# Kernel optimization log

Measured on AMD Instinct MI355X. Metric: run time of the kernel, lower is better.

## Reference

```python
import math
import jax, jax.numpy as jnp
from jax import lax
import numpy as np

NUM_EXPERTS = 8
TOP_K = 2
CAPACITY_FACTOR = 1.25
AUX_COEF = 0.01


def setup_inputs() -> dict:
    key = jax.random.key(0)
    k1, k2, k3, k4, k5 = jax.random.split(key, 5)
    B, T, C, I, E = 4, 2048, 768, 3072, NUM_EXPERTS
    x = jax.random.normal(k1, (B, T, C), dtype=jnp.float32)
    Wr = jax.random.normal(k2, (C, E), dtype=jnp.float32) * 0.02
    Wg = jax.random.normal(k3, (E, C, I), dtype=jnp.float32) * 0.02
    Wu = jax.random.normal(k4, (E, C, I), dtype=jnp.float32) * 0.02
    Wp = jax.random.normal(k5, (E, I, C), dtype=jnp.float32) * 0.02
    return {"x": x, "Wr": Wr, "Wg": Wg, "Wu": Wu, "Wp": Wp}


def reference(x, Wr, Wg, Wu, Wp):
    E, K = NUM_EXPERTS, TOP_K
    B, T, C = x.shape
    N = B * T
    capacity = max(1, math.ceil(CAPACITY_FACTOR * N / E))  # static: 1280
    xf = x.reshape(N, C)

    # --- router ---
    logits = xf @ Wr                                    # [N, E]
    probs = jax.nn.softmax(logits.astype(jnp.float32), axis=-1)
    gates, idx = lax.top_k(probs, K)                    # [N, 2] each
    gates = gates / jnp.clip(jnp.sum(gates, axis=-1, keepdims=True), 1e-9)

    # --- aux load-balancing loss ---
    oh1 = jax.nn.one_hot(idx[:, 0], E, dtype=jnp.int32)  # [N, E]
    oh2 = jax.nn.one_hot(idx[:, 1], E, dtype=jnp.int32)
    importance = probs.mean(axis=0)
    load = (oh1 + oh2).astype(jnp.float32).mean(axis=0) / K
    aux_loss = jnp.sum(importance * load) * E * AUX_COEF

    # --- capacity positions (running rank within each expert) ---
    pos1 = jnp.sum((jnp.cumsum(oh1, axis=0) - 1) * oh1, axis=-1)   # [N]
    mask1 = pos1 < capacity
    slot1 = idx[:, 0] * capacity + pos1
    count1 = jnp.minimum(jnp.sum(oh1, axis=0), capacity)           # [E]
    pos2 = jnp.sum((jnp.cumsum(oh2, axis=0) - 1) * oh2, axis=-1) + count1[idx[:, 1]]
    mask2 = pos2 < capacity
    slot2 = idx[:, 1] * capacity + pos2

    # --- dispatch (scatter into per-expert buffers; OOB slots dropped) ---
    buf = jnp.zeros((E * capacity, C), dtype=x.dtype)
    s1 = jnp.where(mask1, slot1, E * capacity)
    s2 = jnp.where(mask2, slot2, E * capacity)
    buf = buf.at[s1].set(xf, mode='drop')
    buf = buf.at[s2].set(xf, mode='drop')
    ein = buf.reshape(E, capacity, C)

    # --- per-expert swiglu MLP (grouped GEMMs) ---
    gate = jax.nn.silu(jnp.einsum('enc,ech->enh', ein, Wg))
    up = jnp.einsum('enc,ech->enh', ein, Wu)
    out = jnp.einsum('enh,ehc->enc', gate * up, Wp).reshape(E * capacity, C)

    # --- combine (gather back to token order, renormalized gates) ---
    g1 = gates[:, 0] * mask1.astype(jnp.float32)
    g2 = gates[:, 1] * mask2.astype(jnp.float32)
    denom = jnp.clip(g1 + g2, 1e-9)
    g1 = (g1 / denom).astype(x.dtype)
    g2 = (g2 / denom).astype(x.dtype)
    c1 = jnp.clip(slot1, 0, E * capacity - 1)
    c2 = jnp.clip(slot2, 0, E * capacity - 1)
    y = g1[:, None] * out[c1] + g2[:, None] * out[c2]
    return y.reshape(B, T, C), aux_loss
```

## Files before the change

### kernel.cpp

```cpp
#include <hip/hip_runtime.h>
#include <cstdint>
#include <cstddef>

#define NTOK 8192
#define NEXP 8
#define CAP 1280
#define CDIM 768
#define IDIM 3072
#define EROWS (NEXP*CAP)

typedef __attribute__((ext_vector_type(8))) short short8;
typedef __attribute__((ext_vector_type(4))) float f32x4;
typedef __attribute__((ext_vector_type(4))) unsigned short us4;
typedef __attribute__((ext_vector_type(8))) unsigned short us8;

__device__ __forceinline__ unsigned short f2b(float f) {
  unsigned u = __builtin_bit_cast(unsigned, f);
  u += 0x7FFFu + ((u >> 16) & 1u);
  return (unsigned short)(u >> 16);
}
__device__ __forceinline__ float b2f(unsigned short u) {
  return __builtin_bit_cast(float, ((unsigned)u) << 16);
}

__global__ __launch_bounds__(256) void transpose_cvt64(const float* __restrict__ src,
    unsigned short* __restrict__ dst, int R, int S) {
  int tilesS = S >> 6, tilesR = R >> 6;
  int perE = tilesR * tilesS;
  int e = blockIdx.x / perE;
  int rem = blockIdx.x % perE;
  int rt = rem / tilesS, st = rem % tilesS;
  const float* se = src + (size_t)e*R*S + ((size_t)rt*64)*S + st*64;
  unsigned short* de = dst + (size_t)e*R*S + ((size_t)st*64)*R + rt*64;
  __shared__ float tile[64][65];
  int c4 = (threadIdx.x & 15)*4, rr = threadIdx.x >> 4;
#pragma unroll
  for (int p = 0; p < 4; ++p) {
    float4 v = *(const float4*)(se + (size_t)(rr + 16*p)*S + c4);
    tile[rr + 16*p][c4+0] = v.x; tile[rr + 16*p][c4+1] = v.y;
    tile[rr + 16*p][c4+2] = v.z; tile[rr + 16*p][c4+3] = v.w;
  }
  __syncthreads();
#pragma unroll
  for (int p = 0; p < 4; ++p) {
    int s = rr + 16*p;
    us4 o;
    o.x = f2b(tile[c4+0][s]); o.y = f2b(tile[c4+1][s]);
    o.z = f2b(tile[c4+2][s]); o.w = f2b(tile[c4+3][s]);
    *(us4*)(de + (size_t)s*R + c4) = o;
  }
}

__global__ __launch_bounds__(256) void wgu_cvt64(const float* __restrict__ Wg,
    const float* __restrict__ Wu, unsigned short* __restrict__ Wgu) {
  const int tilesR = CDIM/64, tilesS = IDIM/64;
  const int perE = tilesR * tilesS;
  int sel = blockIdx.x / (NEXP*perE);
  int rem = blockIdx.x % (NEXP*perE);
  int e = rem / perE; int r2 = rem % perE;
  int rt = r2 / tilesS, st = r2 % tilesS;
  const float* se = (sel ? Wu : Wg) + (size_t)e*CDIM*IDIM + ((size_t)rt*64)*IDIM + st*64;
  __shared__ float tile[64][65];
  int c4 = (threadIdx.x & 15)*4, rr = threadIdx.x >> 4;
#pragma unroll
  for (int p = 0; p < 4; ++p) {
    float4 v = *(const float4*)(se + (size_t)(rr + 16*p)*IDIM + c4);
    tile[rr + 16*p][c4+0] = v.x; tile[rr + 16*p][c4+1] = v.y;
    tile[rr + 16*p][c4+2] = v.z; tile[rr + 16*p][c4+3] = v.w;
  }
  __syncthreads();
  unsigned short* dstE = Wgu + (size_t)e*(2*IDIM)*CDIM;
#pragma unroll
  for (int p = 0; p < 4; ++p) {
    int s = rr + 16*p;
    int np = 128*st + 32*(s>>4) + (s&15) + sel*16;
    us4 o;
    o.x = f2b(tile[c4+0][s]); o.y = f2b(tile[c4+1][s]);
    o.z = f2b(tile[c4+2][s]); o.w = f2b(tile[c4+3][s]);
    *(us4*)(dstE + (size_t)np*CDIM + rt*64 + c4) = o;
  }
}

__global__ __launch_bounds__(256) void router_kernel(const float* __restrict__ x,
    const float* __restrict__ Wr, float* __restrict__ probs,
    int* __restrict__ idx1, int* __restrict__ idx2,
    float* __restrict__ g1r, float* __restrict__ g2r) {
  __shared__ float WrT[NEXP*CDIM];
  for (int i = threadIdx.x; i < NEXP*CDIM; i += 256) {
    int c = i >> 3, e = i & 7;
    WrT[e*CDIM + c] = Wr[i];
  }
  __syncthreads();
  int w = threadIdx.x >> 6, l = threadIdx.x & 63;
  int t = blockIdx.x*4 + w;
  float acc[NEXP];
#pragma unroll
  for (int e = 0; e < NEXP; ++e) acc[e] = 0.f;
  for (int k = 0; k < CDIM/64; ++k) {
    float xv = x[(size_t)t*CDIM + k*64 + l];
#pragma unroll
    for (int e = 0; e < NEXP; ++e) acc[e] += xv * WrT[e*CDIM + k*64 + l];
  }
#pragma unroll
  for (int off = 32; off > 0; off >>= 1) {
#pragma unroll
    for (int e = 0; e < NEXP; ++e) acc[e] += __shfl_xor(acc[e], off);
  }
  if (l == 0) {
    float m = acc[0];
#pragma unroll
    for (int e = 1; e < NEXP; ++e) m = fmaxf(m, acc[e]);
    float p[NEXP]; float s = 0.f;
#pragma unroll
    for (int e = 0; e < NEXP; ++e) { p[e] = expf(acc[e] - m); s += p[e]; }
    float inv = 1.f / s;
#pragma unroll
    for (int e = 0; e < NEXP; ++e) { p[e] *= inv; probs[(size_t)t*NEXP + e] = p[e]; }
    int i1 = 0; float b1 = p[0];
#pragma unroll
    for (int e = 1; e < NEXP; ++e) if (p[e] > b1) { b1 = p[e]; i1 = e; }
    int i2 = -1; float b2 = -1e30f;
#pragma unroll
    for (int e = 0; e < NEXP; ++e) if (e != i1 && p[e] > b2) { b2 = p[e]; i2 = e; }
    float gs = fmaxf(b1 + b2, 1e-9f);
    g1r[t] = b1 / gs; g2r[t] = b2 / gs;
    idx1[t] = i1; idx2[t] = i2;
  }
}

__global__ __launch_bounds__(1024) void scan_kernel(
    const int* __restrict__ idx1, const int* __restrict__ idx2,
    const float* __restrict__ g1r, const float* __restrict__ g2r,
    const float* __restrict__ probs,
    int* __restrict__ bufmap,
    int* __restrict__ c1o, int* __restrict__ c2o,
    float* __restrict__ g1o, float* __restrict__ g2o,
    float* __restrict__ aux_out) {
  __shared__ unsigned int scanbuf[1024][9];
  __shared__ unsigned int totals[NEXP];
  int tid = threadIdx.x;
  int e1[8], e2[8];
  unsigned int cnt[NEXP];
#pragma unroll
  for (int k = 0; k < NEXP; ++k) cnt[k] = 0;
  for (int j = 0; j < 8; ++j) {
    int t = tid*8 + j;
    e1[j] = idx1[t]; e2[j] = idx2[t];
    cnt[e1[j]] += 1u;
    cnt[e2[j]] += (1u << 16);
  }
#pragma unroll
  for (int k = 0; k < NEXP; ++k) scanbuf[tid][k] = cnt[k];
  unsigned int run[NEXP];
#pragma unroll
  for (int k = 0; k < NEXP; ++k) run[k] = cnt[k];
  __syncthreads();
  for (int off = 1; off < 1024; off <<= 1) {
    unsigned int add[NEXP];
#pragma unroll
    for (int k = 0; k < NEXP; ++k) add[k] = 0;
    if (tid >= off) {
#pragma unroll
      for (int k = 0; k < NEXP; ++k) add[k] = scanbuf[tid - off][k];
    }
    __syncthreads();
#pragma unroll
    for (int k = 0; k < NEXP; ++k) { run[k] += add[k]; scanbuf[tid][k] = run[k]; }
    __syncthreads();
  }
  if (tid == 1023) {
#pragma unroll
    for (int k = 0; k < NEXP; ++k) totals[k] = run[k];
  }
  __syncthreads();
  unsigned int excl[NEXP];
#pragma unroll
  for (int k = 0; k < NEXP; ++k) excl[k] = run[k] - cnt[k];
  int cnt1c[NEXP];
#pragma unroll
  for (int k = 0; k < NEXP; ++k) cnt1c[k] = min((int)(totals[k] & 0xFFFFu), CAP);

  for (int j = 0; j < 8; ++j) {
    int t = tid*8 + j;
    int a = e1[j];
    int pos1 = (int)(excl[a] & 0xFFFFu); excl[a] += 1u;
    int slot1 = a*CAP + pos1;
    bool m1 = pos1 < CAP;
    if (m1) bufmap[slot1] = t;
    int b = e2[j];
    int pos2 = (int)(excl[b] >> 16) + cnt1c[b]; excl[b] += (1u << 16);
    int slot2 = b*CAP + pos2;
    bool m2 = pos2 < CAP;
    if (m2) bufmap[slot2] = t;
    float G1 = m1 ? g1r[t] : 0.f;
    float G2 = m2 ? g2r[t] : 0.f;
    float den = fmaxf(G1 + G2, 1e-9f);
    g1o[t] = G1 / den; g2o[t] = G2 / den;
    c1o[t] = min(slot1, EROWS - 1);
    c2o[t] = min(slot2, EROWS - 1);
  }

  float imp[NEXP];
#pragma unroll
  for (int k = 0; k < NEXP; ++k) imp[k] = 0.f;
  for (int j = 0; j < 8; ++j) {
    int t = tid*8 + j;
    const float4* pr = (const float4*)(probs + (size_t)t*NEXP);
    float4 a0 = pr[0], a1 = pr[1];
    imp[0] += a0.x; imp[1] += a0.y; imp[2] += a0.z; imp[3] += a0.w;
    imp[4] += a1.x; imp[5] += a1.y; imp[6] += a1.z; imp[7] += a1.w;
  }
  __syncthreads();
  float* fbuf = (float*)&scanbuf[0][0];
#pragma unroll
  for (int k = 0; k < NEXP; ++k) fbuf[tid*9 + k] = imp[k];
  __syncthreads();
  for (int s = 512; s >= 1; s >>= 1) {
    if (tid < s) {
#pragma unroll
      for (int k = 0; k < NEXP; ++k) fbuf[tid*9 + k] += fbuf[(tid + s)*9 + k];
    }
    __syncthreads();
  }
  if (tid == 0) {
    float aux = 0.f;
#pragma unroll
    for (int k = 0; k < NEXP; ++k) {
      float importance = fbuf[k] / (float)NTOK;
      float loadk = (float)((totals[k] & 0xFFFFu) + (totals[k] >> 16)) / ((float)NTOK * 2.0f);
      aux += importance * loadk;
    }
    aux_out[0] = aux * (float)NEXP * 0.01f;
  }
}

__global__ __launch_bounds__(192) void dispatch_kernel(const float* __restrict__ x,
    const int* __restrict__ bufmap, unsigned short* __restrict__ ein) {
  int r = blockIdx.x;
  int t = bufmap[r];
  int q = threadIdx.x;
  float4 v = make_float4(0.f, 0.f, 0.f, 0.f);
  if (t >= 0) v = ((const float4*)x)[(size_t)t*(CDIM/4) + q];
  us4 o;
  o.x = f2b(v.x); o.y = f2b(v.y); o.z = f2b(v.z); o.w = f2b(v.w);
  ((us4*)ein)[(size_t)r*(CDIM/4) + q] = o;
}

#define BAR  asm volatile("s_barrier" ::: "memory")
#define VMW(N) asm volatile("s_waitcnt vmcnt(" #N ")" ::: "memory")
#define LGW  asm volatile("s_waitcnt lgkmcnt(0)" ::: "memory")
#define P1 __builtin_amdgcn_s_setprio(1)
#define P0 __builtin_amdgcn_s_setprio(0)

template<int KD>
__global__ __launch_bounds__(512, 2) void gemm1_8ph(
    const unsigned short* __restrict__ A,
    const unsigned short* __restrict__ Bw,
    unsigned short* __restrict__ H) {
  __shared__ unsigned short lds[81920];
  constexpr size_t JSTR = (size_t)6*256*KD;

  const int bid = blockIdx.x;
  const int chunk = gridDim.x >> 3;
  const int tile = (bid & 7)*chunk + (bid >> 3);
  const int e = tile / 30;
  const int r30 = tile % 30;
  const int ntb = r30 / 5, mt = r30 % 5;

  const int tid = threadIdx.x;
  const int l = tid & 63, wid = tid >> 6;
  const int wr = wid >> 2, wc = wid & 3;
  const int lrow = l & 15, khi = l >> 4;

  const unsigned short* Ab = A  + (size_t)e*CAP*KD      + (size_t)mt*256*KD;
  const unsigned short* Bb = Bw + (size_t)e*(2*IDIM)*KD + (size_t)ntb*256*KD;

  const int srow = tid >> 3;
  const int scol = (tid & 7) ^ (srow & 7);
  const size_t lane_off = (size_t)srow*KD + scol*8;
  const int lds_st = wid*512;

#define STG(dstu, srcp, half, kt) do { \
    const unsigned short* s_ = (srcp) + lane_off + (size_t)(half)*128*KD + (size_t)(kt)*64; \
    unsigned short* d_ = (unsigned short*)lds + (dstu) + (half)*8192 + lds_st; \
    __builtin_amdgcn_global_load_lds((const __attribute__((address_space(1))) void*)s_, \
        (__attribute__((address_space(3))) void*)d_, 16, 0, 0); \
    __builtin_amdgcn_global_load_lds((const __attribute__((address_space(1))) void*)(s_ + (size_t)64*KD), \
        (__attribute__((address_space(3))) void*)(d_ + 4096), 16, 0, 0); \
  } while(0)

  const int swz0 = ((khi    ) ^ (lrow & 7)) * 8;
  const int swz1 = ((4 + khi) ^ (lrow & 7)) * 8;
  const int aoff = wr*8192 + lrow*64;
  const int boff = (wc>>1)*8192 + ((wc&1)*64 + lrow)*64;

#define LDA(ab, dst, mb) do { _Pragma("unroll") for (int m_=0;m_<4;++m_) { \
    dst[m_][0] = *(const short8*)(lds + (ab) + aoff + ((mb)+m_)*1024 + swz0); \
    dst[m_][1] = *(const short8*)(lds + (ab) + aoff + ((mb)+m_)*1024 + swz1); } } while(0)
#define LDB(bb, dst, nb) do { _Pragma("unroll") for (int n_=0;n_<2;++n_) { \
    dst[n_][0] = *(const short8*)(lds + (bb) + boff + ((nb)+n_)*1024 + swz0); \
    dst[n_][1] = *(const short8*)(lds + (bb) + boff + ((nb)+n_)*1024 + swz1); } } while(0)
#define QUAD(af, bf, mb, nb) do { _Pragma("unroll") for (int r_=0;r_<2;++r_) \
    _Pragma("unroll") for (int n_=0;n_<2;++n_) \
    _Pragma("unroll") for (int m_=0;m_<4;++m_) \
      acc[(mb)+m_][(nb)+n_] = __builtin_amdgcn_mfma_f32_16x16x32_bf16(af[m_][r_], bf[n_][r_], acc[(mb)+m_][(nb)+n_], 0,0,0); } while(0)

  f32x4 acc[8][4];
#pragma unroll
  for (int i = 0; i < 8; ++i)
#pragma unroll
    for (int j = 0; j < 4; ++j) acc[i][j] = (f32x4){0.f,0.f,0.f,0.f};

  short8 a[4][2], bl[2][2], bh[2][2];

  int bA_ = 32768, bB_ = 49152, bC_ = 65536;

  STG(0, Ab, 0, 0);      STG(bA_, Bb, 0, 0);
  STG(0, Ab, 1, 0);      STG(bA_, Bb, 1, 0);
  STG(16384, Ab, 0, 1);  STG(bB_, Bb, 0, 1);
  STG(16384, Ab, 1, 1);  STG(bB_, Bb, 1, 1);
  VMW(8);
  BAR;

#define ITER(k2p, B2) \
    LDA(0, a, 0); LDB(bA_, bl, 0); STG(bC_, (B2), 0, (k2p)); \
    BAR; P1; QUAD(a, bl, 0, 0); P0; BAR; \
    LDB(bA_, bh, 2); STG(bC_, (B2), 1, (k2p)); \
    BAR; P1; QUAD(a, bh, 0, 2); P0; BAR; \
    LDA(0, a, 4); \
    BAR; P1; QUAD(a, bh, 4, 2); P0; BAR; \
    STG(0, Ab, 0, (k2p)); VMW(6); \
    BAR; P1; QUAD(a, bl, 4, 0); P0; BAR; \
    LDA(16384, a, 0); LDB(bB_, bl, 0); STG(0, Ab, 1, (k2p)); STG(bA_, (B2), 0, (k2p)+1); \
    BAR; P1; QUAD(a, bl, 0, 0); P0; BAR; \
    LDB(bB_, bh, 2); STG(bA_, (B2), 1, (k2p)+1); \
    BAR; P1; QUAD(a, bh, 0, 2); P0; BAR; \
    LDA(16384, a, 4); \
    BAR; P1; QUAD(a, bh, 4, 2); P0; BAR; \
    STG(16384, Ab, 0, (k2p)+1); STG(16384, Ab, 1, (k2p)+1); VMW(8); \
    BAR; P1; QUAD(a, bl, 4, 0); P0; BAR;

  const size_t rowg = (size_t)e*CAP + (size_t)mt*256;
  int itr = 0;

#pragma unroll 1
  for (int j = 0; j < 4; ++j) {
#pragma unroll 1
    for (int ii = 0; ii < 6; ++ii) {
      int t2 = 2*itr + 2;
      if (t2 >= 48) t2 = 0;
      int j2 = t2 / 12, k2 = t2 - j2*12;
      const unsigned short* B2 = Bb + (size_t)j2*JSTR;
      ITER(k2, B2);
      int tmp = bC_; bC_ = bB_; bB_ = bA_; bA_ = tmp;
      ++itr;
    }
    {
      const size_t ntcol = (size_t)(ntb + 6*j)*128;
#pragma unroll
      for (int c = 0; c < 4; ++c) {
        BAR;
        if (wr == (c >> 1)) {
#pragma unroll
          for (int m_ = 0; m_ < 4; ++m_) {
#pragma unroll
            for (int p = 0; p < 2; ++p) {
              f32x4 g = acc[(c & 1)*4 + m_][2*p], u = acc[(c & 1)*4 + m_][2*p+1];
#pragma unroll
              for (int r = 0; r < 4; ++r) {
                float gv = g[r];
                float hv = gv / (1.f + __expf(-gv)) * u[r];
                lds[bC_ + (m_*16 + khi*4 + r)*136 + wc*32 + lrow + p*16] = f2b(hv);
              }
            }
          }
        }
        LGW;
        BAR;
#pragma unroll
        for (int q = 0; q < 2; ++q) {
          int idx = tid + 512*q;
          int rp = idx >> 4, ch = idx & 15;
          us8 v = *(const us8*)(lds + bC_ + rp*136 + ch*8);
          *(us8*)(H + (rowg + 64*c + rp)*(size_t)IDIM + ntcol + ch*8) = v;
        }
      }
      BAR;
    }
#pragma unroll
    for (int i2 = 0; i2 < 8; ++i2)
#pragma unroll
      for (int j2 = 0; j2 < 4; ++j2) acc[i2][j2] = (f32x4){0.f,0.f,0.f,0.f};
  }

#undef ITER
#undef QUAD
#undef LDB
#undef LDA
#undef STG
}

template<int KD>
__global__ __launch_bounds__(512, 2) void gemm2_8ph(
    const unsigned short* __restrict__ A,
    const unsigned short* __restrict__ Bw,
    unsigned short* __restrict__ O) {
  constexpr int NT = KD/64;
  constexpr int NITER = NT/2;
  __shared__ unsigned short lds[57344];

  const int bid = blockIdx.x;
  const int chunk = gridDim.x >> 3;
  const int tile = (bid & 7)*chunk + (bid >> 3);
  const int e = tile / 30;
  const int rem = tile % 30;
  const int nt = rem / 5, mt = rem % 5;

  const int tid = threadIdx.x;
  const int l = tid & 63, wid = tid >> 6;
  const int wr = wid >> 1, wc = wid & 1;
  const int lrow = l & 15, khi = l >> 4;

  const unsigned short* Ab = A  + (size_t)e*CAP*KD  + (size_t)mt*256*KD;
  const unsigned short* Bb = Bw + (size_t)e*CDIM*KD + (size_t)nt*128*KD;

  const int srow = tid >> 3;
  const int scol = (tid & 7) ^ (srow & 7);
  const size_t lane_off = (size_t)srow*KD + scol*8;
  const int lds_st = wid*512;

#define STG(dstu, srcp, half, kt) do { \
    const unsigned short* s_ = (srcp) + lane_off + (size_t)(half)*128*KD + (size_t)(kt)*64; \
    unsigned short* d_ = (unsigned short*)lds + (dstu) + (half)*8192 + lds_st; \
    __builtin_amdgcn_global_load_lds((const __attribute__((address_space(1))) void*)s_, \
        (__attribute__((address_space(3))) void*)d_, 16, 0, 0); \
    __builtin_amdgcn_global_load_lds((const __attribute__((address_space(1))) void*)(s_ + (size_t)64*KD), \
        (__attribute__((address_space(3))) void*)(d_ + 4096), 16, 0, 0); \
  } while(0)

  const int swz0 = ((khi    ) ^ (lrow & 7)) * 8;
  const int swz1 = ((4 + khi) ^ (lrow & 7)) * 8;
  const int aoff = wr*4096 + lrow*64;
  const int boff = wc*4096 + lrow*64;

#define LDA(ab, dst) do { _Pragma("unroll") for (int m_=0;m_<4;++m_) { \
    dst[m_][0] = *(const short8*)(lds + (ab) + aoff + m_*1024 + swz0); \
    dst[m_][1] = *(const short8*)(lds + (ab) + aoff + m_*1024 + swz1); } } while(0)
#define LDB(bb, dst, nb) do { _Pragma("unroll") for (int n_=0;n_<2;++n_) { \
    dst[n_][0] = *(const short8*)(lds + (bb) + boff + ((nb)+n_)*1024 + swz0); \
    dst[n_][1] = *(const short8*)(lds + (bb) + boff + ((nb)+n_)*1024 + swz1); } } while(0)
#define QUAD(af, bf, nb) do { _Pragma("unroll") for (int r_=0;r_<2;++r_) \
    _Pragma("unroll") for (int n_=0;n_<2;++n_) \
    _Pragma("unroll") for (int m_=0;m_<4;++m_) \
      acc[m_][(nb)+n_] = __builtin_amdgcn_mfma_f32_16x16x32_bf16(af[m_][r_], bf[n_][r_], acc[m_][(nb)+n_], 0,0,0); } while(0)

  f32x4 acc[4][4];
#pragma unroll
  for (int i = 0; i < 4; ++i)
#pragma unroll
    for (int j = 0; j < 4; ++j) acc[i][j] = (f32x4){0.f,0.f,0.f,0.f};

  short8 a[4][2], bl[2][2], bh[2][2];

  int bA_ = 32768, bB_ = 40960, bC_ = 49152;

  STG(0, Ab, 0, 0); STG(0, Ab, 1, 0); STG(bA_, Bb, 0, 0);
  STG(16384, Ab, 0, 1); STG(16384, Ab, 1, 1); STG(bB_, Bb, 0, 1);
  VMW(6);
  BAR;

#define ITER2(t2, t3, DOS, VM2, VM4) \
    LDA(0, a); LDB(bA_, bl, 0); if (DOS) STG(bC_, Bb, 0, (t2)); \
    BAR; P1; QUAD(a, bl, 0); P0; BAR; \
    LDB(bA_, bh, 2); if (DOS) { STG(0, Ab, 0, (t2)); STG(0, Ab, 1, (t2)); } VM2; \
    BAR; P1; QUAD(a, bh, 2); P0; BAR; \
    LDA(16384, a); LDB(bB_, bl, 0); if (DOS) STG(bA_, Bb, 0, (t3)); \
    BAR; P1; QUAD(a, bl, 0); P0; BAR; \
    LDB(bB_, bh, 2); if (DOS) { STG(16384, Ab, 0, (t3)); STG(16384, Ab, 1, (t3)); } VM4; \
    BAR; P1; QUAD(a, bh, 2); P0; BAR;

#pragma unroll 1
  for (int i = 0; i < NITER-1; ++i) {
    const int t2 = 2*i+2, t3 = 2*i+3;
    ITER2(t2, t3, true, VMW(6), VMW(6));
    int tmp = bC_; bC_ = bB_; bB_ = bA_; bA_ = tmp;
  }
  ITER2(0, 0, false, VMW(0), VMW(0));

#undef ITER2
#undef QUAD
#undef LDB
#undef LDA
#undef STG

  __syncthreads();
  {
    const int cb0 = wc*64 + lrow;
    const int rb0 = wr*64 + khi*4;
#pragma unroll
    for (int m = 0; m < 4; ++m)
#pragma unroll
      for (int n = 0; n < 4; ++n) {
        f32x4 v = acc[m][n];
#pragma unroll
        for (int r = 0; r < 4; ++r)
          lds[(rb0 + m*16 + r)*136 + cb0 + n*16] = f2b(v[r]);
      }
  }
  __syncthreads();
  const size_t rowg = (size_t)e*CAP + (size_t)mt*256;
  const size_t colg = (size_t)nt*128 + (size_t)(l & 15)*8;
#pragma unroll
  for (int i = 0; i < 8; ++i) {
    int row = wid*32 + i*4 + (l >> 4);
    us8 v = *(const us8*)(lds + row*136 + (l & 15)*8);
    *(us8*)(O + (rowg + row)*(size_t)CDIM + colg) = v;
  }
}

__global__ __launch_bounds__(192) void combine_kernel(const unsigned short* __restrict__ outbuf,
    const int* __restrict__ c1, const int* __restrict__ c2,
    const float* __restrict__ g1, const float* __restrict__ g2,
    float* __restrict__ y) {
  int t = blockIdx.x;
  int q = threadIdx.x;
  float f1 = g1[t], f2 = g2[t];
  int a = c1[t], b = c2[t];
  us4 va = ((const us4*)outbuf)[(size_t)a*(CDIM/4) + q];
  us4 vb = ((const us4*)outbuf)[(size_t)b*(CDIM/4) + q];
  float4 r;
  r.x = f1*b2f(va.x) + f2*b2f(vb.x);
  r.y = f1*b2f(va.y) + f2*b2f(vb.y);
  r.z = f1*b2f(va.z) + f2*b2f(vb.z);
  r.w = f1*b2f(va.w) + f2*b2f(vb.w);
  ((float4*)y)[(size_t)t*(CDIM/4) + q] = r;
}

extern "C" void kernel_launch(void* const* d_in, const int* in_sizes, int n_in,
                              void* d_out, int out_size, void* d_ws, size_t ws_size,
                              hipStream_t stream) {
  const float* x  = (const float*)d_in[0];
  const float* Wr = (const float*)d_in[1];
  const float* Wg = (const float*)d_in[2];
  const float* Wu = (const float*)d_in[3];
  const float* Wp = (const float*)d_in[4];
  float* y = (float*)d_out;

  char* p = (char*)d_ws;
  auto alloc = [&](size_t bytes) { char* r = p; p += (bytes + 255) & ~(size_t)255; return r; };
  unsigned short* WguT = (unsigned short*)alloc((size_t)NEXP*2*IDIM*CDIM*2);
  unsigned short* WpT  = (unsigned short*)alloc((size_t)NEXP*CDIM*IDIM*2);
  unsigned short* ein  = (unsigned short*)alloc((size_t)EROWS*CDIM*2);
  unsigned short* h    = (unsigned short*)alloc((size_t)EROWS*IDIM*2);
  unsigned short* outbuf = (unsigned short*)alloc((size_t)EROWS*CDIM*2);
  float* probs  = (float*)alloc((size_t)NTOK*NEXP*4);
  int* idx1 = (int*)alloc(NTOK*4);
  int* idx2 = (int*)alloc(NTOK*4);
  int* c1   = (int*)alloc(NTOK*4);
  int* c2   = (int*)alloc(NTOK*4);
  float* g1r = (float*)alloc(NTOK*4);
  float* g2r = (float*)alloc(NTOK*4);
  float* g1o = (float*)alloc(NTOK*4);
  float* g2o = (float*)alloc(NTOK*4);
  int* bufmap = (int*)alloc(EROWS*4);

  size_t required = (size_t)(p - (char*)d_ws);
  if (ws_size < required) return;

  hipMemsetAsync(bufmap, 0xFF, EROWS*sizeof(int), stream);

  wgu_cvt64<<<2*NEXP*(CDIM/64)*(IDIM/64), 256, 0, stream>>>(Wg, Wu, WguT);
  transpose_cvt64<<<NEXP*(IDIM/64)*(CDIM/64), 256, 0, stream>>>(Wp, WpT, IDIM, CDIM);

  router_kernel<<<NTOK/4, 256, 0, stream>>>(x, Wr, probs, idx1, idx2, g1r, g2r);
  scan_kernel<<<1, 1024, 0, stream>>>(idx1, idx2, g1r, g2r, probs, bufmap,
                                      c1, c2, g1o, g2o, y + (size_t)NTOK*CDIM);
  dispatch_kernel<<<EROWS, 192, 0, stream>>>(x, bufmap, ein);

  gemm1_8ph<CDIM><<<240, 512, 0, stream>>>(ein, WguT, h);
  gemm2_8ph<IDIM><<<NEXP*5*(CDIM/128), 512, 0, stream>>>(h, WpT, outbuf);

  combine_kernel<<<NTOK, 192, 0, stream>>>(outbuf, c1, c2, g1o, g2o, y);
}
```

Baseline: 291.0 us.

## Shrink gemm1 N-tile to 128 with 4-phase schedule and 4x2 wave grid

Rewrites the gate/up GEMM kernel to use a 256x128 output tile per step instead of 256x256, with a 4x2 wave layout, a halved accumulator array, smaller LDS buffers, and a 4-phase inner iteration in place of the 8-phase one. Each block now walks 8 column groups instead of 4, and the SwiGLU epilogue writes 64-wide column stripes. This lowers register and LDS pressure and may improve occupancy or latency hiding. In exchange, each B load feeds fewer MFMAs, so there is less reuse of A per load and more barriers per unit of compute.

```diff
diff --git a/kernel.cpp b/kernel.cpp
--- a/kernel.cpp
+++ b/kernel.cpp
@@ -253,12 +253,12 @@
 #define P0 __builtin_amdgcn_s_setprio(0)
 
 template<int KD>
-__global__ __launch_bounds__(512, 2) void gemm1_8ph(
+__global__ __launch_bounds__(512, 2) void gemm1_4ph(
     const unsigned short* __restrict__ A,
     const unsigned short* __restrict__ Bw,
     unsigned short* __restrict__ H) {
-  __shared__ unsigned short lds[81920];
-  constexpr size_t JSTR = (size_t)6*256*KD;
+  __shared__ unsigned short lds[57344];
+  constexpr size_t JSTR = (size_t)6*128*KD;
 
   const int bid = blockIdx.x;
   const int chunk = gridDim.x >> 3;
@@ -269,11 +269,11 @@
 
   const int tid = threadIdx.x;
   const int l = tid & 63, wid = tid >> 6;
-  const int wr = wid >> 2, wc = wid & 3;
+  const int wr = wid >> 1, wc = wid & 1;
   const int lrow = l & 15, khi = l >> 4;
 
   const unsigned short* Ab = A  + (size_t)e*CAP*KD      + (size_t)mt*256*KD;
-  const unsigned short* Bb = Bw + (size_t)e*(2*IDIM)*KD + (size_t)ntb*256*KD;
+  const unsigned short* Bb = Bw + (size_t)e*(2*IDIM)*KD + (size_t)ntb*128*KD;
 
   const int srow = tid >> 3;
   const int scol = (tid & 7) ^ (srow & 7);
@@ -291,64 +291,54 @@
 
   const int swz0 = ((khi    ) ^ (lrow & 7)) * 8;
   const int swz1 = ((4 + khi) ^ (lrow & 7)) * 8;
-  const int aoff = wr*8192 + lrow*64;
-  const int boff = (wc>>1)*8192 + ((wc&1)*64 + lrow)*64;
-
-#define LDA(ab, dst, mb) do { _Pragma("unroll") for (int m_=0;m_<4;++m_) { \
-    dst[m_][0] = *(const short8*)(lds + (ab) + aoff + ((mb)+m_)*1024 + swz0); \
-    dst[m_][1] = *(const short8*)(lds + (ab) + aoff + ((mb)+m_)*1024 + swz1); } } while(0)
+  const int aoff = wr*4096 + lrow*64;
+  const int boff = wc*4096 + lrow*64;
+
+#define LDA(ab, dst) do { _Pragma("unroll") for (int m_=0;m_<4;++m_) { \
+    dst[m_][0] = *(const short8*)(lds + (ab) + aoff + m_*1024 + swz0); \
+    dst[m_][1] = *(const short8*)(lds + (ab) + aoff + m_*1024 + swz1); } } while(0)
 #define LDB(bb, dst, nb) do { _Pragma("unroll") for (int n_=0;n_<2;++n_) { \
     dst[n_][0] = *(const short8*)(lds + (bb) + boff + ((nb)+n_)*1024 + swz0); \
     dst[n_][1] = *(const short8*)(lds + (bb) + boff + ((nb)+n_)*1024 + swz1); } } while(0)
-#define QUAD(af, bf, mb, nb) do { _Pragma("unroll") for (int r_=0;r_<2;++r_) \
+#define QUAD(af, bf, nb) do { _Pragma("unroll") for (int r_=0;r_<2;++r_) \
     _Pragma("unroll") for (int n_=0;n_<2;++n_) \
     _Pragma("unroll") for (int m_=0;m_<4;++m_) \
-      acc[(mb)+m_][(nb)+n_] = __builtin_amdgcn_mfma_f32_16x16x32_bf16(af[m_][r_], bf[n_][r_], acc[(mb)+m_][(nb)+n_], 0,0,0); } while(0)
-
-  f32x4 acc[8][4];
-#pragma unroll
-  for (int i = 0; i < 8; ++i)
+      acc[m_][(nb)+n_] = __builtin_amdgcn_mfma_f32_16x16x32_bf16(af[m_][r_], bf[n_][r_], acc[m_][(nb)+n_], 0,0,0); } while(0)
+
+  f32x4 acc[4][4];
+#pragma unroll
+  for (int i = 0; i < 4; ++i)
 #pragma unroll
     for (int j = 0; j < 4; ++j) acc[i][j] = (f32x4){0.f,0.f,0.f,0.f};
 
   short8 a[4][2], bl[2][2], bh[2][2];
 
-  int bA_ = 32768, bB_ = 49152, bC_ = 65536;
-
-  STG(0, Ab, 0, 0);      STG(bA_, Bb, 0, 0);
-  STG(0, Ab, 1, 0);      STG(bA_, Bb, 1, 0);
-  STG(16384, Ab, 0, 1);  STG(bB_, Bb, 0, 1);
-  STG(16384, Ab, 1, 1);  STG(bB_, Bb, 1, 1);
-  VMW(8);
+  int bA_ = 32768, bB_ = 40960, bC_ = 49152;
+
+  STG(0, Ab, 0, 0); STG(0, Ab, 1, 0); STG(bA_, Bb, 0, 0);
+  STG(16384, Ab, 0, 1); STG(16384, Ab, 1, 1); STG(bB_, Bb, 0, 1);
+  VMW(6);
   BAR;
 
 #define ITER(k2p, B2) \
-    LDA(0, a, 0); LDB(bA_, bl, 0); STG(bC_, (B2), 0, (k2p)); \
-    BAR; P1; QUAD(a, bl, 0, 0); P0; BAR; \
-    LDB(bA_, bh, 2); STG(bC_, (B2), 1, (k2p)); \
-    BAR; P1; QUAD(a, bh, 0, 2); P0; BAR; \
-    LDA(0, a, 4); \
-    BAR; P1; QUAD(a, bh, 4, 2); P0; BAR; \
-    STG(0, Ab, 0, (k2p)); VMW(6); \
-    BAR; P1; QUAD(a, bl, 4, 0); P0; BAR; \
-    LDA(16384, a, 0); LDB(bB_, bl, 0); STG(0, Ab, 1, (k2p)); STG(bA_, (B2), 0, (k2p)+1); \
-    BAR; P1; QUAD(a, bl, 0, 0); P0; BAR; \
-    LDB(bB_, bh, 2); STG(bA_, (B2), 1, (k2p)+1); \
-    BAR; P1; QUAD(a, bh, 0, 2); P0; BAR; \
-    LDA(16384, a, 4); \
-    BAR; P1; QUAD(a, bh, 4, 2); P0; BAR; \
-    STG(16384, Ab, 0, (k2p)+1); STG(16384, Ab, 1, (k2p)+1); VMW(8); \
-    BAR; P1; QUAD(a, bl, 4, 0); P0; BAR;
+    LDA(0, a); LDB(bA_, bl, 0); STG(bC_, (B2), 0, (k2p)); \
+    BAR; P1; QUAD(a, bl, 0); P0; BAR; \
+    LDB(bA_, bh, 2); STG(0, Ab, 0, (k2p)); STG(0, Ab, 1, (k2p)); VMW(6); \
+    BAR; P1; QUAD(a, bh, 2); P0; BAR; \
+    LDA(16384, a); LDB(bB_, bl, 0); STG(bA_, (B2), 0, (k2p)+1); \
+    BAR; P1; QUAD(a, bl, 0); P0; BAR; \
+    LDB(bB_, bh, 2); STG(16384, Ab, 0, (k2p)+1); STG(16384, Ab, 1, (k2p)+1); VMW(6); \
+    BAR; P1; QUAD(a, bh, 2); P0; BAR;
 
   const size_t rowg = (size_t)e*CAP + (size_t)mt*256;
   int itr = 0;
 
 #pragma unroll 1
-  for (int j = 0; j < 4; ++j) {
+  for (int j = 0; j < 8; ++j) {
 #pragma unroll 1
     for (int ii = 0; ii < 6; ++ii) {
       int t2 = 2*itr + 2;
-      if (t2 >= 48) t2 = 0;
+      if (t2 >= 96) t2 = 0;
       int j2 = t2 / 12, k2 = t2 - j2*12;
       const unsigned short* B2 = Bb + (size_t)j2*JSTR;
       ITER(k2, B2);
@@ -356,21 +346,22 @@
       ++itr;
     }
     {
-      const size_t ntcol = (size_t)(ntb + 6*j)*128;
-#pragma unroll
-      for (int c = 0; c < 4; ++c) {
+      const size_t ntcol = (size_t)(ntb + 6*j)*64;
+#pragma unroll
+      for (int c = 0; c < 2; ++c) {
         BAR;
-        if (wr == (c >> 1)) {
+        if ((wr >> 1) == c) {
 #pragma unroll
           for (int m_ = 0; m_ < 4; ++m_) {
 #pragma unroll
             for (int p = 0; p < 2; ++p) {
-              f32x4 g = acc[(c & 1)*4 + m_][2*p], u = acc[(c & 1)*4 + m_][2*p+1];
+              f32x4 g = acc[m_][2*p], u = acc[m_][2*p+1];
 #pragma unroll
               for (int r = 0; r < 4; ++r) {
                 float gv = g[r];
                 float hv = gv / (1.f + __expf(-gv)) * u[r];
-                lds[bC_ + (m_*16 + khi*4 + r)*136 + wc*32 + lrow + p*16] = f2b(hv);
+                int rrel = (wr & 1)*64 + m_*16 + khi*4 + r;
+                lds[bC_ + rrel*64 + (2*wc + p)*16 + lrow] = f2b(hv);
               }
             }
           }
@@ -380,15 +371,15 @@
 #pragma unroll
         for (int q = 0; q < 2; ++q) {
           int idx = tid + 512*q;
-          int rp = idx >> 4, ch = idx & 15;
-          us8 v = *(const us8*)(lds + bC_ + rp*136 + ch*8);
-          *(us8*)(H + (rowg + 64*c + rp)*(size_t)IDIM + ntcol + ch*8) = v;
+          int rp = idx >> 3, ch = idx & 7;
+          us8 v = *(const us8*)(lds + bC_ + rp*64 + ch*8);
+          *(us8*)(H + (rowg + 128*c + rp)*(size_t)IDIM + ntcol + ch*8) = v;
         }
       }
       BAR;
     }
 #pragma unroll
-    for (int i2 = 0; i2 < 8; ++i2)
+    for (int i2 = 0; i2 < 4; ++i2)
 #pragma unroll
       for (int j2 = 0; j2 < 4; ++j2) acc[i2][j2] = (f32x4){0.f,0.f,0.f,0.f};
   }
@@ -577,7 +568,7 @@
                                       c1, c2, g1o, g2o, y + (size_t)NTOK*CDIM);
   dispatch_kernel<<<EROWS, 192, 0, stream>>>(x, bufmap, ein);
 
-  gemm1_8ph<CDIM><<<240, 512, 0, stream>>>(ein, WguT, h);
+  gemm1_4ph<CDIM><<<240, 512, 0, stream>>>(ein, WguT, h);
   gemm2_8ph<IDIM><<<NEXP*5*(CDIM/128), 512, 0, stream>>>(h, WpT, outbuf);
 
   combine_kernel<<<NTOK, 192, 0, stream>>>(outbuf, c1, c2, g1o, g2o, y);
```

Result: slower. 307.8 us (+5.8%).
